# Performance work log

Measured on AMD Instinct MI355X. Metric: run time of the kernel, lower is better.

Reference implementation:

```python
import jax, jax.numpy as jnp
import numpy as np

B, C, H, W = 8, 256, 96, 96
CQ = C // 8

def conv1x1(x, w, b):
    # x: (B,C,H,W), w: (O,C), b: (O,)
    return jnp.einsum('bchw,oc->bohw', x, w) + b[None, :, None, None]

def axial_attend(q, k, v):
    # q,k: (B,CQ,H,W); v: (B,C,H,W). Criss-cross attention with masked diagonal
    # on the column (H) branch and joint softmax over H+W logits.
    Hn = q.shape[2]
    e_h = jnp.einsum('bchw,bcgw->bhwg', q, k)            # (B,H,W,H), g = h'
    eye = jnp.eye(Hn, dtype=bool)
    e_h = jnp.where(eye[None, :, None, :], -jnp.inf, e_h)  # mask h'==h (self on column)
    e_w = jnp.einsum('bchw,bchv->bhwv', q, k)            # (B,H,W,W), v = w'
    attn = jax.nn.softmax(jnp.concatenate([e_h, e_w], axis=-1), axis=-1)
    a_h, a_w = attn[..., :Hn], attn[..., Hn:]
    out_h = jnp.einsum('bcgw,bhwg->bchw', v, a_h)
    out_w = jnp.einsum('bchv,bhwv->bchw', v, a_w)
    return out_h + out_w

def setup_inputs() -> dict:
    key = jax.random.key(0)
    ks = jax.random.split(key, 16)
    s = lambda k, shape, scale=1.0: (jax.random.normal(k, shape, dtype=jnp.float32) * scale)
    return {
        'x0': s(ks[0], (B, C, H, W)),
        'x1': s(ks[1], (B, C, H, W)),
        'wq0': s(ks[2], (CQ, C), 0.06), 'bq0': s(ks[3], (CQ,), 0.06),
        'wk0': s(ks[4], (CQ, C), 0.06), 'bk0': s(ks[5], (CQ,), 0.06),
        'wv0': s(ks[6], (C, C), 0.06),  'bv0': s(ks[7], (C,), 0.06),
        'wq1': s(ks[8], (CQ, C), 0.06), 'bq1': s(ks[9], (CQ,), 0.06),
        'wk1': s(ks[10], (CQ, C), 0.06), 'bk1': s(ks[11], (CQ,), 0.06),
        'wv1': s(ks[12], (C, C), 0.06),  'bv1': s(ks[13], (C,), 0.06),
        'gamma': s(ks[14], (1,)),
    }

def reference(x0, x1, wq0, bq0, wk0, bk0, wv0, bv0, wq1, bq1, wk1, bk1, wv1, bv1, gamma):
    q0 = conv1x1(x0, wq0, bq0); k0 = conv1x1(x0, wk0, bk0); v0 = conv1x1(x0, wv0, bv0)
    q1 = conv1x1(x1, wq1, bq1); k1 = conv1x1(x1, wk1, bk1); v1 = conv1x1(x1, wv1, bv1)
    g = gamma[0]
    # stream 0 output: queries from stream 1, keys/values from stream 0
    cat0 = g * axial_attend(q1, k0, v0) + x0
    # stream 1 output: queries from stream 0, keys/values from stream 1
    cat1 = g * axial_attend(q0, k1, v1) + x1
    return (cat0, cat1)
```

## Files before the change

### kernel.cpp

```cpp
#include <hip/hip_runtime.h>
#include <hip/hip_bf16.h>


#define Bn 8
#define Cn 256
#define NHW 9216

typedef unsigned short u16;
typedef __attribute__((ext_vector_type(8))) _Float16 f16x8;
typedef __attribute__((ext_vector_type(4))) float f32x4;

__device__ __forceinline__ float h2f(u16 v) {
  _Float16 h;
  __builtin_memcpy(&h, &v, 2);
  return (float)h;
}
__device__ __forceinline__ u16 f2h(float f) {
  _Float16 h = (_Float16)f;
  u16 v;
  __builtin_memcpy(&v, &h, 2);
  return v;
}

__global__ __launch_bounds__(256) void pack_all(const float* __restrict__ wq, const float* __restrict__ bq,
                                                const float* __restrict__ wk, const float* __restrict__ bk,
                                                const float* __restrict__ wv, const float* __restrict__ bv,
                                                u16* __restrict__ Wall, float* __restrict__ ball) {
  int i = blockIdx.x * 256 + threadIdx.x;
  if (i < 320 * 256) {
    int o = i >> 8, c = i & 255;
    float v = (o < 32) ? wq[o * 256 + c] : (o < 64) ? wk[(o - 32) * 256 + c] : wv[(o - 64) * 256 + c];
    Wall[i] = f2h(v);
  }
  if (i < 320) ball[i] = (i < 32) ? bq[i] : (i < 64) ? bk[i - 32] : bv[i - 64];
}

__global__ __launch_bounds__(256, 2) void proj_all(const float* __restrict__ X, const u16* __restrict__ Wall,
                                                   const float* __restrict__ ball, u16* __restrict__ Pt,
                                                   u16* __restrict__ vW) {
  __shared__ u16 xs[96][264];
  u16* sO = &xs[0][0];
  const int h = blockIdx.x, b = blockIdx.y;
  const int tid = threadIdx.x;
  const float* Xb = X + (size_t)b * Cn * NHW + h * 96;
  for (int idx = tid; idx < 6144; idx += 256) {
    int cin = idx / 24, n4 = idx % 24;
    float4 v = *(const float4*)(Xb + (size_t)cin * NHW + n4 * 4);
    xs[n4 * 4 + 0][cin] = f2h(v.x);
    xs[n4 * 4 + 1][cin] = f2h(v.y);
    xs[n4 * 4 + 2][cin] = f2h(v.z);
    xs[n4 * 4 + 3][cin] = f2h(v.w);
  }
  __syncthreads();
  const int lane = tid & 63, wv = tid >> 6;
  const int arow = lane & 15;
  const int g = lane >> 4;
  const int kc = g * 8;
  f32x4 acc[5][6] = {};
#pragma unroll
  for (int kk = 0; kk < 8; ++kk) {
    f16x8 a5[5], b6[6];
#pragma unroll
    for (int j = 0; j < 5; ++j)
      a5[j] = *(const f16x8*)(Wall + (size_t)((wv + 4 * j) * 16 + arow) * 256 + kk * 32 + kc);
#pragma unroll
    for (int nt = 0; nt < 6; ++nt)
      b6[nt] = *(const f16x8*)&xs[nt * 16 + arow][kk * 32 + kc];
#pragma unroll
    for (int j = 0; j < 5; ++j)
#pragma unroll
      for (int nt = 0; nt < 6; ++nt)
        acc[j][nt] = __builtin_amdgcn_mfma_f32_16x16x32_f16(a5[j], b6[nt], acc[j][nt], 0, 0, 0);
  }
  {
    u16* Ptb = Pt + (size_t)b * ((size_t)NHW * 64);
    float4 bv = *(const float4*)(ball + wv * 16 + (g << 2));
#pragma unroll
    for (int nt = 0; nt < 6; ++nt) {
      int n = h * 96 + nt * 16 + arow;
      f32x4 a = acc[0][nt];
      ushort4 r;
      r.x = f2h(a[0] + bv.x); r.y = f2h(a[1] + bv.y);
      r.z = f2h(a[2] + bv.z); r.w = f2h(a[3] + bv.w);
      *(ushort4*)&Ptb[(size_t)n * 64 + wv * 16 + (g << 2)] = r;
    }
  }
  __syncthreads();
  for (int r = 0; r < 2; ++r) {
#pragma unroll
    for (int jj = 0; jj < 2; ++jj) {
      int j = 2 * r + 1 + jj;
      float4 bv = *(const float4*)(ball + 64 + (j - 1) * 64 + wv * 16 + (g << 2));
      float ba[4] = {bv.x, bv.y, bv.z, bv.w};
#pragma unroll
      for (int nt = 0; nt < 6; ++nt) {
        int col = nt * 16 + arow;
#pragma unroll
        for (int rr = 0; rr < 4; ++rr) {
          int lrow = jj * 64 + wv * 16 + (g << 2) + rr;
          sO[lrow * 104 + col] = f2h(acc[j][nt][rr] + ba[rr]);
        }
      }
    }
    __syncthreads();
    for (int idx = tid; idx < 1536; idx += 256) {
      int cc = idx / 12, c4 = idx % 12;
      *(float4*)(vW + ((size_t)(b * 96 + h) * 256 + r * 128 + cc) * 96 + c4 * 8) =
          *(const float4*)&sO[cc * 104 + c4 * 8];
    }
    __syncthreads();
  }
}

__global__ __launch_bounds__(256) void vtrans(const u16* __restrict__ vW0, const u16* __restrict__ vW1,
                                              u16* __restrict__ vH0, u16* __restrict__ vH1) {
  __shared__ u16 t[96][98];
  const int c = blockIdx.x, b = blockIdx.y;
  const u16* vWp = blockIdx.z ? vW1 : vW0;
  u16* vHp = blockIdx.z ? vH1 : vH0;
  for (int idx = threadIdx.x; idx < 4608; idx += 256) {
    int hh = idx / 48, w2 = idx % 48;
    *(unsigned int*)&t[hh][w2 * 2] =
        *(const unsigned int*)(vWp + (size_t)(b * 96 + hh) * 24576 + c * 96 + w2 * 2);
  }
  __syncthreads();
  for (int idx = threadIdx.x; idx < 4608; idx += 256) {
    int ww = idx / 48, g2 = idx % 48;
    unsigned int lo = t[g2 * 2][ww];
    unsigned int hi = t[g2 * 2 + 1][ww];
    *(unsigned int*)(vHp + (size_t)(b * 96 + ww) * 24576 + c * 96 + g2 * 2) = lo | (hi << 16);
  }
}

__global__ __launch_bounds__(384, 3) void attn_fused(const u16* __restrict__ Qpt, const u16* __restrict__ Kpt,
                                                     const u16* __restrict__ vWp, const u16* __restrict__ vHp,
                                                     float* __restrict__ mW, float* __restrict__ sW,
                                                     float* __restrict__ mH, float* __restrict__ sH,
                                                     u16* __restrict__ tmpW, u16* __restrict__ tmpH) {
  __shared__ __align__(16) char smem[46592];
  u16* vbuf = (u16*)smem;
  u16* qs = (u16*)smem;
  u16* ks = (u16*)(smem + 7680);
  u16* probs = (u16*)(smem + 26624);
  const int p = blockIdx.x, b = blockIdx.y, z = blockIdx.z;
  const int tid = threadIdx.x;
  const size_t nbase = (size_t)b * ((size_t)NHW * 64);
  const size_t rowoff = z ? (size_t)p * 64 : (size_t)p * 6144;
  const int rstride = z ? 6144 : 64;
  for (int idx = tid; idx < 768; idx += 384) {
    int i = idx >> 3, c8 = idx & 7;
    const u16* src = (c8 < 4)
        ? Qpt + nbase + rowoff + (size_t)i * rstride + c8 * 8
        : Kpt + nbase + rowoff + (size_t)i * rstride + 32 + (c8 - 4) * 8;
    float4 v = *(const float4*)src;
    u16* dst = (c8 < 4) ? &qs[i * 40 + c8 * 8] : &ks[i * 40 + (c8 - 4) * 8];
    *(float4*)dst = v;
  }
  __syncthreads();
  const int lane = tid & 63, wv = tid >> 6;
  const int cl = lane & 15, g = lane >> 4;
  const int kc = g * 8;
  f32x4 eacc[6];
  {
    f16x8 aq = *(const f16x8*)&qs[(wv * 16 + cl) * 40 + kc];
#pragma unroll
    for (int nt = 0; nt < 6; ++nt) {
      f16x8 bk = *(const f16x8*)&ks[(nt * 16 + cl) * 40 + kc];
      f32x4 zz = {0.f, 0.f, 0.f, 0.f};
      eacc[nt] = __builtin_amdgcn_mfma_f32_16x16x32_f16(aq, bk, zz, 0, 0, 0);
    }
  }
  float mx[4], sm[4];
#pragma unroll
  for (int r = 0; r < 4; ++r) {
    int i = wv * 16 + 4 * g + r;
    float m = -1e30f;
#pragma unroll
    for (int nt = 0; nt < 6; ++nt) {
      float e = eacc[nt][r];
      if (z && (nt * 16 + cl) == i) { e = -1e30f; eacc[nt][r] = e; }
      m = fmaxf(m, e);
    }
    m = fmaxf(m, __shfl_xor(m, 1));
    m = fmaxf(m, __shfl_xor(m, 2));
    m = fmaxf(m, __shfl_xor(m, 4));
    m = fmaxf(m, __shfl_xor(m, 8));
    float s = 0.f;
#pragma unroll
    for (int nt = 0; nt < 6; ++nt) {
      float pv = __expf(eacc[nt][r] - m);
      eacc[nt][r] = pv;
      s += pv;
    }
    s += __shfl_xor(s, 1);
    s += __shfl_xor(s, 2);
    s += __shfl_xor(s, 4);
    s += __shfl_xor(s, 8);
    mx[r] = m; sm[r] = s;
  }
#pragma unroll
  for (int r = 0; r < 4; ++r) {
    int i = wv * 16 + 4 * g + r;
#pragma unroll
    for (int nt = 0; nt < 6; ++nt)
      probs[i * 104 + nt * 16 + cl] = f2h(eacc[nt][r]);
    if (cl == 0) {
      size_t sidx = z ? ((size_t)(b * 96 + i) * 96 + p) : ((size_t)(b * 96 + p) * 96 + i);
      (z ? mH : mW)[sidx] = mx[r];
      (z ? sH : sW)[sidx] = sm[r];
    }
  }
  __syncthreads();
  const u16* Vp = z ? vHp : vWp;
  u16* tOut = z ? tmpH : tmpW;
  const int w0 = wv * 16;
  f16x8 af[3];
#pragma unroll
  for (int kt = 0; kt < 3; ++kt)
    af[kt] = *(const f16x8*)&probs[(w0 + cl) * 104 + kt * 32 + kc];
  const size_t vbase = (size_t)(b * 96 + p) * 24576;
  for (int half = 0; half < 2; ++half) {
    for (int idx = tid; idx < 1536; idx += 384) {
      int r = idx / 12, c4 = idx % 12;
      *(float4*)&vbuf[r * 104 + c4 * 8] = *(const float4*)(Vp + vbase + (size_t)(half * 128 + r) * 96 + c4 * 8);
    }
    __syncthreads();
    f32x4 acc[8];
#pragma unroll
    for (int nt = 0; nt < 8; ++nt) {
      f32x4 a = {0.f, 0.f, 0.f, 0.f};
#pragma unroll
      for (int kt = 0; kt < 3; ++kt) {
        f16x8 bf = *(const f16x8*)&vbuf[(nt * 16 + cl) * 104 + kt * 32 + kc];
        a = __builtin_amdgcn_mfma_f32_16x16x32_f16(af[kt], bf, a, 0, 0, 0);
      }
      acc[nt] = a;
    }
    __syncthreads();
#pragma unroll
    for (int nt = 0; nt < 8; ++nt) {
      int c2 = nt * 16 + cl;
      int wr = w0 + (g << 2);
#pragma unroll
      for (int r = 0; r < 4; ++r) vbuf[c2 * 104 + wr + r] = f2h(acc[nt][r]);
    }
    __syncthreads();
    for (int idx = tid; idx < 1536; idx += 384) {
      int r = idx / 12, c4 = idx % 12;
      *(float4*)(tOut + vbase + (size_t)(half * 128 + r) * 96 + c4 * 8) = *(const float4*)&vbuf[r * 104 + c4 * 8];
    }
    __syncthreads();
  }
}

__global__ __launch_bounds__(256) void scl_k(const float* __restrict__ mH, const float* __restrict__ sH,
                                             const float* __restrict__ mW, const float* __restrict__ sW,
                                             const float* __restrict__ gammaP, float* __restrict__ sclH,
                                             float* __restrict__ sclW) {
  int i = blockIdx.x * 256 + threadIdx.x;
  if (i >= Bn * 9216) return;
  float mh = mH[i], mw = mW[i];
  float m = fmaxf(mh, mw);
  float eh = __expf(mh - m), ew = __expf(mw - m);
  float s = sH[i] * eh + sW[i] * ew;
  float g = gammaP[0] / s;
  sclH[i] = g * eh;
  sclW[i] = g * ew;
}

__global__ __launch_bounds__(256) void tkomb(const u16* __restrict__ tmpH, const u16* __restrict__ tmpW,
                                             const float* __restrict__ x, const float* __restrict__ sclH,
                                             const float* __restrict__ sclW, float* __restrict__ out) {
  __shared__ u16 t[96][108];
  const int c = blockIdx.x, b = blockIdx.y;
  const int tid = threadIdx.x;
  for (int idx = tid; idx < 2304; idx += 256) {
    int w_ = idx / 24, h4 = idx % 24;
    *(ushort4*)&t[w_][h4 * 4] =
        *(const ushort4*)(tmpH + ((size_t)(b * 96 + w_) * 256 + c) * 96 + h4 * 4);
  }
  __syncthreads();
  for (int idx = tid; idx < 2304; idx += 256) {
    int h_ = idx / 24, w4 = idx % 24;
    size_t go = ((size_t)(b * 256 + c) * 96 + h_) * 96 + w4 * 4;
    float4 xv = *(const float4*)(x + go);
    ushort4 wvv = *(const ushort4*)(tmpW + ((size_t)(b * 96 + h_) * 256 + c) * 96 + w4 * 4);
    float4 sh4 = *(const float4*)(sclH + (size_t)(b * 96 + h_) * 96 + w4 * 4);
    float4 sw4 = *(const float4*)(sclW + (size_t)(b * 96 + h_) * 96 + w4 * 4);
    float4 ov;
    ov.x = xv.x + h2f(t[w4 * 4 + 0][h_]) * sh4.x + h2f(wvv.x) * sw4.x;
    ov.y = xv.y + h2f(t[w4 * 4 + 1][h_]) * sh4.y + h2f(wvv.y) * sw4.y;
    ov.z = xv.z + h2f(t[w4 * 4 + 2][h_]) * sh4.z + h2f(wvv.z) * sw4.z;
    ov.w = xv.w + h2f(t[w4 * 4 + 3][h_]) * sh4.w + h2f(wvv.w) * sw4.w;
    *(float4*)(out + go) = ov;
  }
}

extern "C" void kernel_launch(void* const* d_in, const int* in_sizes, int n_in,
                              void* d_out, int out_size, void* d_ws, size_t ws_size,
                              hipStream_t stream) {
  const float* x0 = (const float*)d_in[0];
  const float* x1 = (const float*)d_in[1];
  const float* wq0 = (const float*)d_in[2];
  const float* bq0 = (const float*)d_in[3];
  const float* wk0 = (const float*)d_in[4];
  const float* bk0 = (const float*)d_in[5];
  const float* wv0 = (const float*)d_in[6];
  const float* bv0 = (const float*)d_in[7];
  const float* wq1 = (const float*)d_in[8];
  const float* bq1 = (const float*)d_in[9];
  const float* wk1 = (const float*)d_in[10];
  const float* bk1 = (const float*)d_in[11];
  const float* wv1 = (const float*)d_in[12];
  const float* bv1 = (const float*)d_in[13];
  const float* gamma = (const float*)d_in[14];
  float* out = (float*)d_out;

  char* ws = (char*)d_ws;
  size_t off = 0;
  auto alloc = [&](size_t bytes) -> void* {
    void* ptr = ws + off;
    off += (bytes + 255) & ~(size_t)255;
    return ptr;
  };
  const size_t SZ_P = (size_t)Bn * NHW * 64 * 2;
  const size_t SZ_V = (size_t)Bn * NHW * Cn * 2;
  const size_t SZ_S = (size_t)Bn * 9216 * 4;
  u16* Pt0 = (u16*)alloc(SZ_P);
  u16* Pt1 = (u16*)alloc(SZ_P);
  u16* vW0 = (u16*)alloc(SZ_V);
  u16* vW1 = (u16*)alloc(SZ_V);
  u16* vH0 = (u16*)alloc(SZ_V);
  u16* vH1 = (u16*)alloc(SZ_V);
  u16* tmpW = (u16*)alloc(SZ_V);
  u16* tmpH = (u16*)alloc(SZ_V);
  u16* Wall0 = (u16*)alloc(320 * 256 * 2);
  u16* Wall1 = (u16*)alloc(320 * 256 * 2);
  float* ball0 = (float*)alloc(320 * 4);
  float* ball1 = (float*)alloc(320 * 4);
  float* mH = (float*)alloc(SZ_S);
  float* sH = (float*)alloc(SZ_S);
  float* mW = (float*)alloc(SZ_S);
  float* sW = (float*)alloc(SZ_S);
  float* sclH = (float*)alloc(SZ_S);
  float* sclW = (float*)alloc(SZ_S);
  (void)ws_size; (void)in_sizes; (void)n_in; (void)out_size;

  pack_all<<<320, 256, 0, stream>>>(wq0, bq0, wk0, bk0, wv0, bv0, Wall0, ball0);
  pack_all<<<320, 256, 0, stream>>>(wq1, bq1, wk1, bk1, wv1, bv1, Wall1, ball1);

  dim3 gp(96, Bn), gc(256, Bn), gt(256, Bn, 2), ga(96, Bn, 2);
  proj_all<<<gp, 256, 0, stream>>>(x0, Wall0, ball0, Pt0, vW0);
  proj_all<<<gp, 256, 0, stream>>>(x1, Wall1, ball1, Pt1, vW1);
  vtrans<<<gt, 256, 0, stream>>>(vW0, vW1, vH0, vH1);

  attn_fused<<<ga, 384, 0, stream>>>(Pt1, Pt0, vW0, vH0, mW, sW, mH, sH, tmpW, tmpH);
  scl_k<<<288, 256, 0, stream>>>(mH, sH, mW, sW, gamma, sclH, sclW);
  tkomb<<<gc, 256, 0, stream>>>(tmpH, tmpW, x0, sclH, sclW, out);

  attn_fused<<<ga, 384, 0, stream>>>(Pt0, Pt1, vW1, vH1, mW, sW, mH, sH, tmpW, tmpH);
  scl_k<<<288, 256, 0, stream>>>(mH, sH, mW, sW, gamma, sclH, sclW);
  tkomb<<<gc, 256, 0, stream>>>(tmpH, tmpW, x1, sclH, sclW, out + (size_t)Bn * Cn * NHW);
}
```

Baseline: 342.2 us.

## Load Q/K/V MFMA fragments directly from global, drop LDS staging

The attention kernel no longer stages Q, K and V tiles in shared memory. Each wave now loads its MFMA operand fragments straight from global memory and writes 4-element output chunks directly, instead of transposing through an LDS buffer. Only the probability tile stays in LDS, which removes several barriers and shrinks shared memory use, so more blocks can be resident. The cost is less coalesced global traffic, since loads are 16-byte per lane with strided rows and stores are 8-byte, plus repeated reads of V across waves that now rely on the cache.

```diff
diff --git a/kernel.cpp b/kernel.cpp
--- a/kernel.cpp
+++ b/kernel.cpp
@@ -132,48 +132,33 @@
   }
 }
 
-__global__ __launch_bounds__(384, 3) void attn_fused(const u16* __restrict__ Qpt, const u16* __restrict__ Kpt,
-                                                     const u16* __restrict__ vWp, const u16* __restrict__ vHp,
-                                                     float* __restrict__ mW, float* __restrict__ sW,
-                                                     float* __restrict__ mH, float* __restrict__ sH,
-                                                     u16* __restrict__ tmpW, u16* __restrict__ tmpH) {
-  __shared__ __align__(16) char smem[46592];
-  u16* vbuf = (u16*)smem;
-  u16* qs = (u16*)smem;
-  u16* ks = (u16*)(smem + 7680);
-  u16* probs = (u16*)(smem + 26624);
+__global__ __launch_bounds__(384) void attn_fused(const u16* __restrict__ Qpt, const u16* __restrict__ Kpt,
+                                                  const u16* __restrict__ vWp, const u16* __restrict__ vHp,
+                                                  float* __restrict__ mW, float* __restrict__ sW,
+                                                  float* __restrict__ mH, float* __restrict__ sH,
+                                                  u16* __restrict__ tmpW, u16* __restrict__ tmpH) {
+  __shared__ u16 probs[96 * 104];
   const int p = blockIdx.x, b = blockIdx.y, z = blockIdx.z;
   const int tid = threadIdx.x;
-  const size_t nbase = (size_t)b * ((size_t)NHW * 64);
-  const size_t rowoff = z ? (size_t)p * 64 : (size_t)p * 6144;
-  const int rstride = z ? 6144 : 64;
-  for (int idx = tid; idx < 768; idx += 384) {
-    int i = idx >> 3, c8 = idx & 7;
-    const u16* src = (c8 < 4)
-        ? Qpt + nbase + rowoff + (size_t)i * rstride + c8 * 8
-        : Kpt + nbase + rowoff + (size_t)i * rstride + 32 + (c8 - 4) * 8;
-    float4 v = *(const float4*)src;
-    u16* dst = (c8 < 4) ? &qs[i * 40 + c8 * 8] : &ks[i * 40 + (c8 - 4) * 8];
-    *(float4*)dst = v;
-  }
-  __syncthreads();
   const int lane = tid & 63, wv = tid >> 6;
   const int cl = lane & 15, g = lane >> 4;
   const int kc = g * 8;
+  const int w0 = wv * 16;
+  const size_t base = (size_t)b * ((size_t)NHW * 64) + (size_t)p * (z ? 64 : 6144);
+  const size_t istride = z ? 6144 : 64;
   f32x4 eacc[6];
   {
-    f16x8 aq = *(const f16x8*)&qs[(wv * 16 + cl) * 40 + kc];
+    f16x8 aq = *(const f16x8*)(Qpt + base + (size_t)(w0 + cl) * istride + kc);
 #pragma unroll
     for (int nt = 0; nt < 6; ++nt) {
-      f16x8 bk = *(const f16x8*)&ks[(nt * 16 + cl) * 40 + kc];
+      f16x8 bk = *(const f16x8*)(Kpt + base + (size_t)(nt * 16 + cl) * istride + 32 + kc);
       f32x4 zz = {0.f, 0.f, 0.f, 0.f};
       eacc[nt] = __builtin_amdgcn_mfma_f32_16x16x32_f16(aq, bk, zz, 0, 0, 0);
     }
   }
-  float mx[4], sm[4];
 #pragma unroll
   for (int r = 0; r < 4; ++r) {
-    int i = wv * 16 + 4 * g + r;
+    int i = w0 + 4 * g + r;
     float m = -1e30f;
 #pragma unroll
     for (int nt = 0; nt < 6; ++nt) {
@@ -196,60 +181,35 @@
     s += __shfl_xor(s, 2);
     s += __shfl_xor(s, 4);
     s += __shfl_xor(s, 8);
-    mx[r] = m; sm[r] = s;
-  }
-#pragma unroll
-  for (int r = 0; r < 4; ++r) {
-    int i = wv * 16 + 4 * g + r;
 #pragma unroll
     for (int nt = 0; nt < 6; ++nt)
       probs[i * 104 + nt * 16 + cl] = f2h(eacc[nt][r]);
     if (cl == 0) {
       size_t sidx = z ? ((size_t)(b * 96 + i) * 96 + p) : ((size_t)(b * 96 + p) * 96 + i);
-      (z ? mH : mW)[sidx] = mx[r];
-      (z ? sH : sW)[sidx] = sm[r];
+      (z ? mH : mW)[sidx] = m;
+      (z ? sH : sW)[sidx] = s;
     }
   }
   __syncthreads();
   const u16* Vp = z ? vHp : vWp;
   u16* tOut = z ? tmpH : tmpW;
-  const int w0 = wv * 16;
+  const size_t vbase = (size_t)(b * 96 + p) * 24576;
   f16x8 af[3];
 #pragma unroll
   for (int kt = 0; kt < 3; ++kt)
     af[kt] = *(const f16x8*)&probs[(w0 + cl) * 104 + kt * 32 + kc];
-  const size_t vbase = (size_t)(b * 96 + p) * 24576;
-  for (int half = 0; half < 2; ++half) {
-    for (int idx = tid; idx < 1536; idx += 384) {
-      int r = idx / 12, c4 = idx % 12;
-      *(float4*)&vbuf[r * 104 + c4 * 8] = *(const float4*)(Vp + vbase + (size_t)(half * 128 + r) * 96 + c4 * 8);
-    }
-    __syncthreads();
-    f32x4 acc[8];
-#pragma unroll
-    for (int nt = 0; nt < 8; ++nt) {
-      f32x4 a = {0.f, 0.f, 0.f, 0.f};
-#pragma unroll
-      for (int kt = 0; kt < 3; ++kt) {
-        f16x8 bf = *(const f16x8*)&vbuf[(nt * 16 + cl) * 104 + kt * 32 + kc];
-        a = __builtin_amdgcn_mfma_f32_16x16x32_f16(af[kt], bf, a, 0, 0, 0);
-      }
-      acc[nt] = a;
-    }
-    __syncthreads();
-#pragma unroll
-    for (int nt = 0; nt < 8; ++nt) {
-      int c2 = nt * 16 + cl;
-      int wr = w0 + (g << 2);
-#pragma unroll
-      for (int r = 0; r < 4; ++r) vbuf[c2 * 104 + wr + r] = f2h(acc[nt][r]);
-    }
-    __syncthreads();
-    for (int idx = tid; idx < 1536; idx += 384) {
-      int r = idx / 12, c4 = idx % 12;
-      *(float4*)(tOut + vbase + (size_t)(half * 128 + r) * 96 + c4 * 8) = *(const float4*)&vbuf[r * 104 + c4 * 8];
-    }
-    __syncthreads();
+#pragma unroll
+  for (int nt = 0; nt < 16; ++nt) {
+    const int c = nt * 16 + cl;
+    f32x4 a = {0.f, 0.f, 0.f, 0.f};
+#pragma unroll
+    for (int kt = 0; kt < 3; ++kt) {
+      f16x8 bf = *(const f16x8*)(Vp + vbase + (size_t)c * 96 + kt * 32 + kc);
+      a = __builtin_amdgcn_mfma_f32_16x16x32_f16(af[kt], bf, a, 0, 0, 0);
+    }
+    ushort4 r4;
+    r4.x = f2h(a[0]); r4.y = f2h(a[1]); r4.z = f2h(a[2]); r4.w = f2h(a[3]);
+    *(ushort4*)(tOut + vbase + (size_t)c * 96 + w0 + 4 * g) = r4;
   }
 }
 
```

New measurement: 396.9 us. 16.0% more time.

## Batch both attention streams into single launches and split projection across 512 threads

Applied to the files above, without the earlier changes.

Merges the per-stream launches of pack, projection, attention, scaling and combine kernels into single launches that index the stream with an extra grid dimension. Intermediate buffers are duplicated per stream so both can run concurrently. The projection kernel moves to 512 threads, with waves split across the N dimension and half as many accumulators per wave, to raise occupancy. This removes launch overhead and tail effects of small grids at the cost of more workspace memory and possibly more register or LDS pressure per CU.

```diff
diff --git a/kernel.cpp b/kernel.cpp
--- a/kernel.cpp
+++ b/kernel.cpp
@@ -5,6 +5,7 @@
 #define Bn 8
 #define Cn 256
 #define NHW 9216
+#define PT_BS ((size_t)NHW * 64)
 
 typedef unsigned short u16;
 typedef __attribute__((ext_vector_type(8))) _Float16 f16x8;
@@ -22,10 +23,23 @@
   return v;
 }
 
-__global__ __launch_bounds__(256) void pack_all(const float* __restrict__ wq, const float* __restrict__ bq,
-                                                const float* __restrict__ wk, const float* __restrict__ bk,
-                                                const float* __restrict__ wv, const float* __restrict__ bv,
-                                                u16* __restrict__ Wall, float* __restrict__ ball) {
+__global__ __launch_bounds__(256) void pack_all(const float* __restrict__ wq0, const float* __restrict__ bq0,
+                                                const float* __restrict__ wk0, const float* __restrict__ bk0,
+                                                const float* __restrict__ wv0, const float* __restrict__ bv0,
+                                                const float* __restrict__ wq1, const float* __restrict__ bq1,
+                                                const float* __restrict__ wk1, const float* __restrict__ bk1,
+                                                const float* __restrict__ wv1, const float* __restrict__ bv1,
+                                                u16* __restrict__ Wall0, float* __restrict__ ball0,
+                                                u16* __restrict__ Wall1, float* __restrict__ ball1) {
+  const int pr = blockIdx.y;
+  const float* wq = pr ? wq1 : wq0;
+  const float* bq = pr ? bq1 : bq0;
+  const float* wk = pr ? wk1 : wk0;
+  const float* bk = pr ? bk1 : bk0;
+  const float* wv = pr ? wv1 : wv0;
+  const float* bv = pr ? bv1 : bv0;
+  u16* Wall = pr ? Wall1 : Wall0;
+  float* ball = pr ? ball1 : ball0;
   int i = blockIdx.x * 256 + threadIdx.x;
   if (i < 320 * 256) {
     int o = i >> 8, c = i & 255;
@@ -35,15 +49,22 @@
   if (i < 320) ball[i] = (i < 32) ? bq[i] : (i < 64) ? bk[i - 32] : bv[i - 64];
 }
 
-__global__ __launch_bounds__(256, 2) void proj_all(const float* __restrict__ X, const u16* __restrict__ Wall,
-                                                   const float* __restrict__ ball, u16* __restrict__ Pt,
-                                                   u16* __restrict__ vW) {
+__global__ __launch_bounds__(512, 4) void proj_all(const float* __restrict__ X0, const float* __restrict__ X1,
+                                                   const u16* __restrict__ Wall0, const u16* __restrict__ Wall1,
+                                                   const float* __restrict__ ball0, const float* __restrict__ ball1,
+                                                   u16* __restrict__ Pt0, u16* __restrict__ Pt1,
+                                                   u16* __restrict__ vW0, u16* __restrict__ vW1) {
   __shared__ u16 xs[96][264];
   u16* sO = &xs[0][0];
-  const int h = blockIdx.x, b = blockIdx.y;
+  const int h = blockIdx.x, b = blockIdx.y, pr = blockIdx.z;
+  const float* X = pr ? X1 : X0;
+  const u16* Wall = pr ? Wall1 : Wall0;
+  const float* ball = pr ? ball1 : ball0;
+  u16* Pt = pr ? Pt1 : Pt0;
+  u16* vW = pr ? vW1 : vW0;
   const int tid = threadIdx.x;
   const float* Xb = X + (size_t)b * Cn * NHW + h * 96;
-  for (int idx = tid; idx < 6144; idx += 256) {
+  for (int idx = tid; idx < 6144; idx += 512) {
     int cin = idx / 24, n4 = idx % 24;
     float4 v = *(const float4*)(Xb + (size_t)cin * NHW + n4 * 4);
     xs[n4 * 4 + 0][cin] = f2h(v.x);
@@ -53,36 +74,37 @@
   }
   __syncthreads();
   const int lane = tid & 63, wv = tid >> 6;
+  const int mg = wv >> 1, ng = wv & 1;
   const int arow = lane & 15;
   const int g = lane >> 4;
   const int kc = g * 8;
-  f32x4 acc[5][6] = {};
+  f32x4 acc[5][3] = {};
 #pragma unroll
   for (int kk = 0; kk < 8; ++kk) {
-    f16x8 a5[5], b6[6];
+    f16x8 a5[5], b3[3];
 #pragma unroll
     for (int j = 0; j < 5; ++j)
-      a5[j] = *(const f16x8*)(Wall + (size_t)((wv + 4 * j) * 16 + arow) * 256 + kk * 32 + kc);
-#pragma unroll
-    for (int nt = 0; nt < 6; ++nt)
-      b6[nt] = *(const f16x8*)&xs[nt * 16 + arow][kk * 32 + kc];
+      a5[j] = *(const f16x8*)(Wall + (size_t)((mg + 4 * j) * 16 + arow) * 256 + kk * 32 + kc);
+#pragma unroll
+    for (int nt = 0; nt < 3; ++nt)
+      b3[nt] = *(const f16x8*)&xs[ng * 48 + nt * 16 + arow][kk * 32 + kc];
 #pragma unroll
     for (int j = 0; j < 5; ++j)
 #pragma unroll
-      for (int nt = 0; nt < 6; ++nt)
-        acc[j][nt] = __builtin_amdgcn_mfma_f32_16x16x32_f16(a5[j], b6[nt], acc[j][nt], 0, 0, 0);
+      for (int nt = 0; nt < 3; ++nt)
+        acc[j][nt] = __builtin_amdgcn_mfma_f32_16x16x32_f16(a5[j], b3[nt], acc[j][nt], 0, 0, 0);
   }
   {
-    u16* Ptb = Pt + (size_t)b * ((size_t)NHW * 64);
-    float4 bv = *(const float4*)(ball + wv * 16 + (g << 2));
-#pragma unroll
-    for (int nt = 0; nt < 6; ++nt) {
-      int n = h * 96 + nt * 16 + arow;
+    u16* Ptb = Pt + (size_t)b * PT_BS;
+    float4 bv = *(const float4*)(ball + mg * 16 + (g << 2));
+#pragma unroll
+    for (int nt = 0; nt < 3; ++nt) {
+      int n = h * 96 + ng * 48 + nt * 16 + arow;
       f32x4 a = acc[0][nt];
       ushort4 r;
       r.x = f2h(a[0] + bv.x); r.y = f2h(a[1] + bv.y);
       r.z = f2h(a[2] + bv.z); r.w = f2h(a[3] + bv.w);
-      *(ushort4*)&Ptb[(size_t)n * 64 + wv * 16 + (g << 2)] = r;
+      *(ushort4*)&Ptb[(size_t)n * 64 + mg * 16 + (g << 2)] = r;
     }
   }
   __syncthreads();
@@ -90,20 +112,20 @@
 #pragma unroll
     for (int jj = 0; jj < 2; ++jj) {
       int j = 2 * r + 1 + jj;
-      float4 bv = *(const float4*)(ball + 64 + (j - 1) * 64 + wv * 16 + (g << 2));
+      int vt = mg + 8 * r + 4 * jj;
+      float4 bv = *(const float4*)(ball + 64 + vt * 16 + (g << 2));
       float ba[4] = {bv.x, bv.y, bv.z, bv.w};
-#pragma unroll
-      for (int nt = 0; nt < 6; ++nt) {
-        int col = nt * 16 + arow;
-#pragma unroll
-        for (int rr = 0; rr < 4; ++rr) {
-          int lrow = jj * 64 + wv * 16 + (g << 2) + rr;
-          sO[lrow * 104 + col] = f2h(acc[j][nt][rr] + ba[rr]);
-        }
+      int lrow0 = (mg + 4 * jj) * 16 + (g << 2);
+#pragma unroll
+      for (int nt = 0; nt < 3; ++nt) {
+        int col = ng * 48 + nt * 16 + arow;
+#pragma unroll
+        for (int rr = 0; rr < 4; ++rr)
+          sO[(lrow0 + rr) * 104 + col] = f2h(acc[j][nt][rr] + ba[rr]);
       }
     }
     __syncthreads();
-    for (int idx = tid; idx < 1536; idx += 256) {
+    for (int idx = tid; idx < 1536; idx += 512) {
       int cc = idx / 12, c4 = idx % 12;
       *(float4*)(vW + ((size_t)(b * 96 + h) * 256 + r * 128 + cc) * 96 + c4 * 8) =
           *(const float4*)&sO[cc * 104 + c4 * 8];
@@ -132,21 +154,30 @@
   }
 }
 
-__global__ __launch_bounds__(384, 3) void attn_fused(const u16* __restrict__ Qpt, const u16* __restrict__ Kpt,
-                                                     const u16* __restrict__ vWp, const u16* __restrict__ vHp,
-                                                     float* __restrict__ mW, float* __restrict__ sW,
-                                                     float* __restrict__ mH, float* __restrict__ sH,
-                                                     u16* __restrict__ tmpW, u16* __restrict__ tmpH) {
+__global__ __launch_bounds__(384, 3) void attn_fused(const u16* __restrict__ Pt0, const u16* __restrict__ Pt1,
+                                                     const u16* __restrict__ vW0, const u16* __restrict__ vH0,
+                                                     const u16* __restrict__ vW1, const u16* __restrict__ vH1,
+                                                     float* __restrict__ mWs, float* __restrict__ sWs,
+                                                     float* __restrict__ mHs, float* __restrict__ sHs,
+                                                     u16* __restrict__ tmpW0, u16* __restrict__ tmpH0,
+                                                     u16* __restrict__ tmpW1, u16* __restrict__ tmpH1) {
   __shared__ __align__(16) char smem[46592];
   u16* vbuf = (u16*)smem;
   u16* qs = (u16*)smem;
   u16* ks = (u16*)(smem + 7680);
   u16* probs = (u16*)(smem + 26624);
   const int p = blockIdx.x, b = blockIdx.y, z = blockIdx.z;
+  const int pass = z & 1, pair = z >> 1;
+  const u16* Qpt = pair ? Pt0 : Pt1;
+  const u16* Kpt = pair ? Pt1 : Pt0;
+  const u16* Vp = pair ? (pass ? vH1 : vW1) : (pass ? vH0 : vW0);
+  u16* tOut = pair ? (pass ? tmpH1 : tmpW1) : (pass ? tmpH0 : tmpW0);
+  float* mOut = (pass ? mHs : mWs) + (size_t)pair * (Bn * 9216);
+  float* sOut = (pass ? sHs : sWs) + (size_t)pair * (Bn * 9216);
   const int tid = threadIdx.x;
-  const size_t nbase = (size_t)b * ((size_t)NHW * 64);
-  const size_t rowoff = z ? (size_t)p * 64 : (size_t)p * 6144;
-  const int rstride = z ? 6144 : 64;
+  const size_t nbase = (size_t)b * PT_BS;
+  const size_t rowoff = pass ? (size_t)p * 64 : (size_t)p * 6144;
+  const int rstride = pass ? 6144 : 64;
   for (int idx = tid; idx < 768; idx += 384) {
     int i = idx >> 3, c8 = idx & 7;
     const u16* src = (c8 < 4)
@@ -160,9 +191,10 @@
   const int lane = tid & 63, wv = tid >> 6;
   const int cl = lane & 15, g = lane >> 4;
   const int kc = g * 8;
+  const int w0 = wv * 16;
   f32x4 eacc[6];
   {
-    f16x8 aq = *(const f16x8*)&qs[(wv * 16 + cl) * 40 + kc];
+    f16x8 aq = *(const f16x8*)&qs[(w0 + cl) * 40 + kc];
 #pragma unroll
     for (int nt = 0; nt < 6; ++nt) {
       f16x8 bk = *(const f16x8*)&ks[(nt * 16 + cl) * 40 + kc];
@@ -170,15 +202,14 @@
       eacc[nt] = __builtin_amdgcn_mfma_f32_16x16x32_f16(aq, bk, zz, 0, 0, 0);
     }
   }
-  float mx[4], sm[4];
 #pragma unroll
   for (int r = 0; r < 4; ++r) {
-    int i = wv * 16 + 4 * g + r;
+    int i = w0 + 4 * g + r;
     float m = -1e30f;
 #pragma unroll
     for (int nt = 0; nt < 6; ++nt) {
       float e = eacc[nt][r];
-      if (z && (nt * 16 + cl) == i) { e = -1e30f; eacc[nt][r] = e; }
+      if (pass && (nt * 16 + cl) == i) { e = -1e30f; eacc[nt][r] = e; }
       m = fmaxf(m, e);
     }
     m = fmaxf(m, __shfl_xor(m, 1));
@@ -196,24 +227,16 @@
     s += __shfl_xor(s, 2);
     s += __shfl_xor(s, 4);
     s += __shfl_xor(s, 8);
-    mx[r] = m; sm[r] = s;
-  }
-#pragma unroll
-  for (int r = 0; r < 4; ++r) {
-    int i = wv * 16 + 4 * g + r;
 #pragma unroll
     for (int nt = 0; nt < 6; ++nt)
       probs[i * 104 + nt * 16 + cl] = f2h(eacc[nt][r]);
     if (cl == 0) {
-      size_t sidx = z ? ((size_t)(b * 96 + i) * 96 + p) : ((size_t)(b * 96 + p) * 96 + i);
-      (z ? mH : mW)[sidx] = mx[r];
-      (z ? sH : sW)[sidx] = sm[r];
-    }
-  }
-  __syncthreads();
-  const u16* Vp = z ? vHp : vWp;
-  u16* tOut = z ? tmpH : tmpW;
-  const int w0 = wv * 16;
+      size_t sidx = pass ? ((size_t)(b * 96 + i) * 96 + p) : ((size_t)(b * 96 + p) * 96 + i);
+      mOut[sidx] = m;
+      sOut[sidx] = s;
+    }
+  }
+  __syncthreads();
   f16x8 af[3];
 #pragma unroll
   for (int kt = 0; kt < 3; ++kt)
@@ -222,7 +245,8 @@
   for (int half = 0; half < 2; ++half) {
     for (int idx = tid; idx < 1536; idx += 384) {
       int r = idx / 12, c4 = idx % 12;
-      *(float4*)&vbuf[r * 104 + c4 * 8] = *(const float4*)(Vp + vbase + (size_t)(half * 128 + r) * 96 + c4 * 8);
+      *(float4*)&vbuf[r * 104 + c4 * 8] =
+          *(const float4*)(Vp + vbase + (size_t)(half * 128 + r) * 96 + c4 * 8);
     }
     __syncthreads();
     f32x4 acc[8];
@@ -247,7 +271,8 @@
     __syncthreads();
     for (int idx = tid; idx < 1536; idx += 384) {
       int r = idx / 12, c4 = idx % 12;
-      *(float4*)(tOut + vbase + (size_t)(half * 128 + r) * 96 + c4 * 8) = *(const float4*)&vbuf[r * 104 + c4 * 8];
+      *(float4*)(tOut + vbase + (size_t)(half * 128 + r) * 96 + c4 * 8) =
+          *(const float4*)&vbuf[r * 104 + c4 * 8];
     }
     __syncthreads();
   }
@@ -258,7 +283,7 @@
                                              const float* __restrict__ gammaP, float* __restrict__ sclH,
                                              float* __restrict__ sclW) {
   int i = blockIdx.x * 256 + threadIdx.x;
-  if (i >= Bn * 9216) return;
+  if (i >= 2 * Bn * 9216) return;
   float mh = mH[i], mw = mW[i];
   float m = fmaxf(mh, mw);
   float eh = __expf(mh - m), ew = __expf(mw - m);
@@ -268,11 +293,19 @@
   sclW[i] = g * ew;
 }
 
-__global__ __launch_bounds__(256) void tkomb(const u16* __restrict__ tmpH, const u16* __restrict__ tmpW,
-                                             const float* __restrict__ x, const float* __restrict__ sclH,
-                                             const float* __restrict__ sclW, float* __restrict__ out) {
+__global__ __launch_bounds__(256) void tkomb(const u16* __restrict__ tmpH0, const u16* __restrict__ tmpW0,
+                                             const u16* __restrict__ tmpH1, const u16* __restrict__ tmpW1,
+                                             const float* __restrict__ x0, const float* __restrict__ x1,
+                                             const float* __restrict__ sclH, const float* __restrict__ sclW,
+                                             float* __restrict__ out) {
   __shared__ u16 t[96][108];
-  const int c = blockIdx.x, b = blockIdx.y;
+  const int c = blockIdx.x, b = blockIdx.y, pr = blockIdx.z;
+  const u16* tmpH = pr ? tmpH1 : tmpH0;
+  const u16* tmpW = pr ? tmpW1 : tmpW0;
+  const float* x = pr ? x1 : x0;
+  const float* sH = sclH + (size_t)pr * (Bn * 9216);
+  const float* sW = sclW + (size_t)pr * (Bn * 9216);
+  float* o = out + (size_t)pr * Bn * Cn * NHW;
   const int tid = threadIdx.x;
   for (int idx = tid; idx < 2304; idx += 256) {
     int w_ = idx / 24, h4 = idx % 24;
@@ -285,14 +318,14 @@
     size_t go = ((size_t)(b * 256 + c) * 96 + h_) * 96 + w4 * 4;
     float4 xv = *(const float4*)(x + go);
     ushort4 wvv = *(const ushort4*)(tmpW + ((size_t)(b * 96 + h_) * 256 + c) * 96 + w4 * 4);
-    float4 sh4 = *(const float4*)(sclH + (size_t)(b * 96 + h_) * 96 + w4 * 4);
-    float4 sw4 = *(const float4*)(sclW + (size_t)(b * 96 + h_) * 96 + w4 * 4);
+    float4 sh4 = *(const float4*)(sH + (size_t)(b * 96 + h_) * 96 + w4 * 4);
+    float4 sw4 = *(const float4*)(sW + (size_t)(b * 96 + h_) * 96 + w4 * 4);
     float4 ov;
     ov.x = xv.x + h2f(t[w4 * 4 + 0][h_]) * sh4.x + h2f(wvv.x) * sw4.x;
     ov.y = xv.y + h2f(t[w4 * 4 + 1][h_]) * sh4.y + h2f(wvv.y) * sw4.y;
     ov.z = xv.z + h2f(t[w4 * 4 + 2][h_]) * sh4.z + h2f(wvv.z) * sw4.z;
     ov.w = xv.w + h2f(t[w4 * 4 + 3][h_]) * sh4.w + h2f(wvv.w) * sw4.w;
-    *(float4*)(out + go) = ov;
+    *(float4*)(o + go) = ov;
   }
 }
 
@@ -332,33 +365,30 @@
   u16* vW1 = (u16*)alloc(SZ_V);
   u16* vH0 = (u16*)alloc(SZ_V);
   u16* vH1 = (u16*)alloc(SZ_V);
-  u16* tmpW = (u16*)alloc(SZ_V);
-  u16* tmpH = (u16*)alloc(SZ_V);
+  u16* tmpW0 = (u16*)alloc(SZ_V);
+  u16* tmpH0 = (u16*)alloc(SZ_V);
+  u16* tmpW1 = (u16*)alloc(SZ_V);
+  u16* tmpH1 = (u16*)alloc(SZ_V);
   u16* Wall0 = (u16*)alloc(320 * 256 * 2);
   u16* Wall1 = (u16*)alloc(320 * 256 * 2);
   float* ball0 = (float*)alloc(320 * 4);
   float* ball1 = (float*)alloc(320 * 4);
-  float* mH = (float*)alloc(SZ_S);
-  float* sH = (float*)alloc(SZ_S);
-  float* mW = (float*)alloc(SZ_S);
-  float* sW = (float*)alloc(SZ_S);
-  float* sclH = (float*)alloc(SZ_S);
-  float* sclW = (float*)alloc(SZ_S);
+  float* mH = (float*)alloc(2 * SZ_S);
+  float* sH = (float*)alloc(2 * SZ_S);
+  float* mW = (float*)alloc(2 * SZ_S);
+  float* sW = (float*)alloc(2 * SZ_S);
+  float* sclH = (float*)alloc(2 * SZ_S);
+  float* sclW = (float*)alloc(2 * SZ_S);
   (void)ws_size; (void)in_sizes; (void)n_in; (void)out_size;
 
-  pack_all<<<320, 256, 0, stream>>>(wq0, bq0, wk0, bk0, wv0, bv0, Wall0, ball0);
-  pack_all<<<320, 256, 0, stream>>>(wq1, bq1, wk1, bk1, wv1, bv1, Wall1, ball1);
-
-  dim3 gp(96, Bn), gc(256, Bn), gt(256, Bn, 2), ga(96, Bn, 2);
-  proj_all<<<gp, 256, 0, stream>>>(x0, Wall0, ball0, Pt0, vW0);
-  proj_all<<<gp, 256, 0, stream>>>(x1, Wall1, ball1, Pt1, vW1);
+  dim3 gpk(320, 2), gp(96, Bn, 2), gt(256, Bn, 2), ga(96, Bn, 4), gc(256, Bn, 2);
+  pack_all<<<gpk, 256, 0, stream>>>(wq0, bq0, wk0, bk0, wv0, bv0,
+                                    wq1, bq1, wk1, bk1, wv1, bv1,
+                                    Wall0, ball0, Wall1, ball1);
+  proj_all<<<gp, 512, 0, stream>>>(x0, x1, Wall0, Wall1, ball0, ball1, Pt0, Pt1, vW0, vW1);
   vtrans<<<gt, 256, 0, stream>>>(vW0, vW1, vH0, vH1);
-
-  attn_fused<<<ga, 384, 0, stream>>>(Pt1, Pt0, vW0, vH0, mW, sW, mH, sH, tmpW, tmpH);
-  scl_k<<<288, 256, 0, stream>>>(mH, sH, mW, sW, gamma, sclH, sclW);
-  tkomb<<<gc, 256, 0, stream>>>(tmpH, tmpW, x0, sclH, sclW, out);
-
-  attn_fused<<<ga, 384, 0, stream>>>(Pt0, Pt1, vW1, vH1, mW, sW, mH, sH, tmpW, tmpH);
-  scl_k<<<288, 256, 0, stream>>>(mH, sH, mW, sW, gamma, sclH, sclW);
-  tkomb<<<gc, 256, 0, stream>>>(tmpH, tmpW, x1, sclH, sclW, out + (size_t)Bn * Cn * NHW);
-}
+  attn_fused<<<ga, 384, 0, stream>>>(Pt0, Pt1, vW0, vH0, vW1, vH1,
+                                     mW, sW, mH, sH, tmpW0, tmpH0, tmpW1, tmpH1);
+  scl_k<<<576, 256, 0, stream>>>(mH, sH, mW, sW, gamma, sclH, sclW);
+  tkomb<<<gc, 256, 0, stream>>>(tmpH0, tmpW0, tmpH1, tmpW1, x0, x1, sclH, sclW, out);
+}
```

Measured after the change: 321.0 us. 1.07x faster.
